# Kernel tuning notes

Hardware: AMD Instinct MI355X
Metric: run time of the kernel (lower is better)

Reference implementation:

```python
import jax, jax.numpy as jnp
import numpy as np

NUM_HEADS = 32
MULTI_HOP_MAX_DIST = 20


def setup_inputs() -> dict:
    key = jax.random.key(0)
    ks = jax.random.split(key, 10)
    B, N, D, F = 16, 64, 20, 3
    H = NUM_HEADS
    attn_bias = jax.random.normal(ks[0], (B, N + 1, N + 1), jnp.float32)
    spatial_pos = jax.random.randint(ks[1], (B, N, N), 0, 512)
    x = jax.random.randint(ks[2], (B, N, 9), 0, 512)
    edge_input = jax.random.randint(ks[3], (B, N, N, D, F), 0, 1536)
    attn_edge_type = jax.random.randint(ks[4], (B, N, N, F), 0, 1536)
    mask_2d = jnp.ones((B,), jnp.float32)
    edge_enc_w = (jax.random.normal(ks[5], (1537, H), jnp.float32) * 0.02).at[0].set(0.0)
    edge_dis_enc_w = jax.random.normal(ks[6], (131072, 1), jnp.float32) * 0.02
    spatial_enc_w = (jax.random.normal(ks[7], (512, H), jnp.float32) * 0.02).at[0].set(0.0)
    token_w = jax.random.normal(ks[8], (1, H), jnp.float32) * 0.02
    return {
        'attn_bias': attn_bias, 'spatial_pos': spatial_pos, 'x': x,
        'edge_input': edge_input, 'attn_edge_type': attn_edge_type,
        'mask_2d': mask_2d, 'edge_enc_w': edge_enc_w,
        'edge_dis_enc_w': edge_dis_enc_w, 'spatial_enc_w': spatial_enc_w,
        'token_w': token_w,
    }


def reference(attn_bias, spatial_pos, x, edge_input, attn_edge_type, mask_2d,
              edge_enc_w, edge_dis_enc_w, spatial_enc_w, token_w):
    H = NUM_HEADS
    D = MULTI_HOP_MAX_DIST
    B, N = x.shape[:2]

    # graph_attn_bias: [B, H, N+1, N+1]
    gab = jnp.tile(attn_bias[:, None], (1, H, 1, 1))

    # spatial position bias: gather + permute to [B, H, N, N]
    spb = jnp.transpose(spatial_enc_w[spatial_pos], (0, 3, 1, 2))
    spb = spb * mask_2d[:, None, None, None]
    gab = gab.at[:, :, 1:, 1:].add(spb)

    # virtual-distance token bias on graph-token row/col
    tok = token_w.reshape(1, H, 1)
    gab = gab.at[:, :, 1:, 0].add(tok)
    gab = gab.at[:, :, 0, :].add(tok)

    # spatial_pos_ = clamp(where(sp>1, sp-1, where(sp==0,1,sp)), 0, D)
    sp_ = jnp.where(spatial_pos == 0, 1, spatial_pos)
    sp_ = jnp.where(sp_ > 1, sp_ - 1, sp_)
    sp_ = jnp.clip(sp_, 0, D)

    # multi-hop edge features: [B,N,N,D,F] -> gather -> mean over F -> [B,N,N,D,H]
    ei = edge_input[:, :, :, :D, :]
    ef = edge_enc_w[ei].mean(-2)
    # per-distance head-mixing bmm: [D, B*N*N, H] x [D, H, H]
    flat = jnp.transpose(ef, (3, 0, 1, 2, 4)).reshape(D, -1, H)
    Wd = edge_dis_enc_w.reshape(-1, H, H)[:D]
    flat = jnp.matmul(flat, Wd)
    eb = jnp.transpose(flat.reshape(D, B, N, N, H), (1, 2, 3, 0, 4))
    eb = eb.sum(-2) / sp_.astype(jnp.float32)[..., None]  # [B,N,N,H]
    eb = jnp.transpose(eb, (0, 3, 1, 2)) * mask_2d[:, None, None, None]
    gab = gab.at[:, :, 1:, 1:].add(eb)

    return gab + attn_bias[:, None]
```

## Files before the change

### kernel.cpp

```cpp
#include <hip/hip_runtime.h>
#include <hip/hip_bf16.h>

#define NH 32
#define NV 1537
#define ND 20
#define NB 16
#define NN 64

#define ENCP_U32 (NV*10)
#define WD8_U32  (ND*NH*8)

#define CVT1_BLOCKS ((NV*8 + 255)/256)
#define CVT2_BLOCKS (WD8_U32/256)

#define MAIN_LDS 61480

typedef unsigned int   u32;
typedef unsigned short u16;
typedef __attribute__((ext_vector_type(4))) float        f32x4;
typedef __attribute__((ext_vector_type(4))) unsigned int u32x4;
typedef __attribute__((ext_vector_type(4))) int          v4i;

__device__ __forceinline__ u32 f32x4_to_fp8(float a0, float a1, float a2, float a3) {
#if __has_builtin(__builtin_amdgcn_cvt_pk_fp8_f32)
    u32 u = __builtin_amdgcn_cvt_pk_fp8_f32(a0, a1, 0u, false);
    u     = __builtin_amdgcn_cvt_pk_fp8_f32(a2, a3, u,  true);
    return u;
#else
    u32 lo, hi;
    asm("v_cvt_pk_fp8_f32 %0, %1, %2" : "=v"(lo) : "v"(a0), "v"(a1));
    asm("v_cvt_pk_fp8_f32 %0, %1, %2" : "=v"(hi) : "v"(a2), "v"(a3));
    return (lo & 0xffffu) | (hi << 16);
#endif
}

__global__ void __launch_bounds__(256)
prep_kernel(const float* __restrict__ enc,
            const float* __restrict__ wdis,
            u32* __restrict__ tab) {
    int blk = blockIdx.x, tid = threadIdx.x;
    if (blk < CVT1_BLOCKS) {
        int o = blk * 256 + tid;
        if (o < NV * 8) {
            float4 e = *(const float4*)(enc + (size_t)o * 4);
            tab[(o >> 3) * 10 + (o & 7)] = f32x4_to_fp8(e.x * 256.f, e.y * 256.f,
                                                        e.z * 256.f, e.w * 256.f);
        }
    } else {
        int o = (blk - CVT1_BLOCKS) * 256 + tid;
        int d = o >> 8, rem = o & 255;
        int h = rem >> 3, k4 = rem & 7;
        const float* ws = wdis + d * 1024 + h;
        tab[ENCP_U32 + (d * 32 + h) * 8 + k4] =
            f32x4_to_fp8(ws[(k4 * 4 + 0) * 32] * 256.f,
                         ws[(k4 * 4 + 1) * 32] * 256.f,
                         ws[(k4 * 4 + 2) * 32] * 256.f,
                         ws[(k4 * 4 + 3) * 32] * 256.f);
    }
}

__global__ void __launch_bounds__(512, 4)
main_kernel(const float* __restrict__ ab,
            const int*   __restrict__ spos,
            const int*   __restrict__ eidx,
            const float* __restrict__ mask2d,
            const float* __restrict__ spw,
            const float* __restrict__ tokw,
            const u32*   __restrict__ tab,
            float*       __restrict__ out) {
    extern __shared__ __align__(16) char dyn[];

    int tid = threadIdx.x, blk = blockIdx.x;
    int b = blk >> 5, i0 = (blk & 31) << 1;

    int wv = tid >> 6, l = tid & 63;
    int c16 = l & 15, g = l >> 4;
    int cellLoc = wv * 16 + c16;

    const int* ep = eidx + ((size_t)blk * 128 + cellLoc) * 60;
    u32 w[30];
#pragma unroll
    for (int k = 0; k < 15; ++k) {
        v4i q = *(const v4i*)(ep + k * 4);
        w[2 * k]     = ((u32)q.x & 0xffffu) | ((u32)q.y << 16);
        w[2 * k + 1] = ((u32)q.z & 0xffffu) | ((u32)q.w << 16);
    }

    {
        const u32x4* g4 = (const u32x4*)tab;
        u32x4* s4 = (u32x4*)dyn;
        for (int p = tid; p < 3842; p += 512) s4[p] = g4[p];
        if (tid < 2) ((u32*)dyn)[15368 + tid] = tab[15368 + tid];
    }
    __syncthreads();

    const char* encB = dyn + g * 8;
    const u32* wdg = tab + ENCP_U32;

    f32x4 acc[2][3] = {};

#pragma unroll
    for (int d = 0; d < ND; ++d) {
        u32 q0 = (w[(3 * d    ) >> 1] >> (((3 * d    ) & 1) * 16)) & 0xffffu;
        u32 q1 = (w[(3 * d + 1) >> 1] >> (((3 * d + 1) & 1) * 16)) & 0xffffu;
        u32 q2 = (w[(3 * d + 2) >> 1] >> (((3 * d + 2) & 1) * 16)) & 0xffffu;
        long bf0 = *(const long*)(wdg + (d * 32 + c16) * 8 + g * 2);
        long bf1 = *(const long*)(wdg + (d * 32 + c16 + 16) * 8 + g * 2);
        long a0 = *(const long*)(encB + q0 * 40u);
        long a1 = *(const long*)(encB + q1 * 40u);
        long a2 = *(const long*)(encB + q2 * 40u);
        acc[0][0] = __builtin_amdgcn_mfma_f32_16x16x32_fp8_fp8(a0, bf0, acc[0][0], 0, 0, 0);
        acc[1][0] = __builtin_amdgcn_mfma_f32_16x16x32_fp8_fp8(a0, bf1, acc[1][0], 0, 0, 0);
        acc[0][1] = __builtin_amdgcn_mfma_f32_16x16x32_fp8_fp8(a1, bf0, acc[0][1], 0, 0, 0);
        acc[1][1] = __builtin_amdgcn_mfma_f32_16x16x32_fp8_fp8(a1, bf1, acc[1][1], 0, 0, 0);
        acc[0][2] = __builtin_amdgcn_mfma_f32_16x16x32_fp8_fp8(a2, bf0, acc[0][2], 0, 0, 0);
        acc[1][2] = __builtin_amdgcn_mfma_f32_16x16x32_fp8_fp8(a2, bf1, acc[1][2], 0, 0, 0);
    }
    f32x4 acc0 = acc[0][0] + acc[0][1] + acc[0][2];
    f32x4 acc1 = acc[1][0] + acc[1][1] + acc[1][2];

    __syncthreads();
    float* comb = (float*)dyn;
    float m = mask2d[b];
#pragma unroll
    for (int r = 0; r < 4; ++r) {
        int cell = wv * 16 + g * 4 + r;
        int s = spos[blk * 128 + cell];
        int sp = (s == 0) ? 1 : s;
        sp = (sp > 1) ? sp - 1 : sp;
        sp = (sp > ND) ? ND : sp;
        float esc = m / (196608.0f * (float)sp);
        float spbL = spw[s * NH + c16];
        float spbH = spw[s * NH + c16 + 16];
        comb[cell * 33 + c16]      = spbL * m + acc0[r] * esc;
        comb[cell * 33 + c16 + 16] = spbH * m + acc1[r] * esc;
    }
    __syncthreads();

#pragma unroll
    for (int w8 = 0; w8 < 8; ++w8) {
        int idx = w8 * 512 + tid;
        int j = idx & 63, h = (idx >> 6) & 31, r = idx >> 11;
        float av = ab[(b * 65 + i0 + r + 1) * 65 + (j + 1)];
        __builtin_nontemporal_store(2.0f * av + comb[(r * 64 + j) * 33 + h],
            &out[(((size_t)b * NH + h) * 65 + i0 + r + 1) * 65 + (j + 1)]);
    }

    if (tid < 2 * NH) {
        int r = tid >> 5, h = tid & 31;
        float av0 = ab[(b * 65 + i0 + r + 1) * 65];
        __builtin_nontemporal_store(2.0f * av0 + tokw[h],
            &out[(((size_t)b * NH + h) * 65 + i0 + r + 1) * 65 + 0]);
    }
    if (i0 == 0) {
        for (int t = tid; t < NH * 65; t += 512) {
            int h = t / 65, j = t - h * 65;
            __builtin_nontemporal_store(2.0f * ab[b * 4225 + j] + tokw[h],
                &out[(((size_t)b * NH + h) * 65 + 0) * 65 + j]);
        }
    }
}

extern "C" void kernel_launch(void* const* d_in, const int* in_sizes, int n_in,
                              void* d_out, int out_size, void* d_ws, size_t ws_size,
                              hipStream_t stream) {
    const float* attn_bias   = (const float*)d_in[0];
    const int*   spatial_pos = (const int*)  d_in[1];
    const int*   edge_input  = (const int*)  d_in[3];
    const float* mask_2d     = (const float*)d_in[5];
    const float* edge_enc_w  = (const float*)d_in[6];
    const float* edge_dis_w  = (const float*)d_in[7];
    const float* spatial_w   = (const float*)d_in[8];
    const float* token_w     = (const float*)d_in[9];
    float* out = (float*)d_out;
    u32* tab = (u32*)d_ws;

    prep_kernel<<<CVT1_BLOCKS + CVT2_BLOCKS, 256, 0, stream>>>(
        edge_enc_w, edge_dis_w, tab);
    main_kernel<<<512, 512, MAIN_LDS, stream>>>(attn_bias, spatial_pos, edge_input,
                                                mask_2d, spatial_w, token_w,
                                                tab, out);
}
```

Baseline: 23.05 us.

## Drop LDS row padding, load edge indices in-loop, raise occupancy target

Stores the fp8 edge-encoding table with a dense 32-byte row stride instead of 40 bytes, which shrinks LDS per block and lets the row offset be computed with a shift. The up-front edge-index prefetch into 30 packed registers is removed; indices are now read from global memory inside the unrolled distance loop. Launch bounds are raised from 4 to 6 blocks per CU to trade registers for occupancy. Risks: a 32-byte stride can cause LDS bank conflicts on the gathers, and loading indices late exposes global memory latency right before each MFMA.

```diff
diff --git a/kernel.cpp b/kernel.cpp
--- a/kernel.cpp
+++ b/kernel.cpp
@@ -7,19 +7,18 @@
 #define NB 16
 #define NN 64
 
-#define ENCP_U32 (NV*10)
-#define WD8_U32  (ND*NH*8)
+#define ENC_U32 (NV*8)
+#define WD8_U32 (ND*NH*8)
 
-#define CVT1_BLOCKS ((NV*8 + 255)/256)
+#define CVT1_BLOCKS ((ENC_U32 + 255)/256)
 #define CVT2_BLOCKS (WD8_U32/256)
 
-#define MAIN_LDS 61480
+#define MAIN_LDS 49184
 
 typedef unsigned int   u32;
 typedef unsigned short u16;
 typedef __attribute__((ext_vector_type(4))) float        f32x4;
 typedef __attribute__((ext_vector_type(4))) unsigned int u32x4;
-typedef __attribute__((ext_vector_type(4))) int          v4i;
 
 __device__ __forceinline__ u32 f32x4_to_fp8(float a0, float a1, float a2, float a3) {
 #if __has_builtin(__builtin_amdgcn_cvt_pk_fp8_f32)
@@ -41,17 +40,17 @@
     int blk = blockIdx.x, tid = threadIdx.x;
     if (blk < CVT1_BLOCKS) {
         int o = blk * 256 + tid;
-        if (o < NV * 8) {
+        if (o < ENC_U32) {
             float4 e = *(const float4*)(enc + (size_t)o * 4);
-            tab[(o >> 3) * 10 + (o & 7)] = f32x4_to_fp8(e.x * 256.f, e.y * 256.f,
-                                                        e.z * 256.f, e.w * 256.f);
+            tab[o] = f32x4_to_fp8(e.x * 256.f, e.y * 256.f,
+                                  e.z * 256.f, e.w * 256.f);
         }
     } else {
         int o = (blk - CVT1_BLOCKS) * 256 + tid;
         int d = o >> 8, rem = o & 255;
         int h = rem >> 3, k4 = rem & 7;
         const float* ws = wdis + d * 1024 + h;
-        tab[ENCP_U32 + (d * 32 + h) * 8 + k4] =
+        tab[ENC_U32 + (d * 32 + h) * 8 + k4] =
             f32x4_to_fp8(ws[(k4 * 4 + 0) * 32] * 256.f,
                          ws[(k4 * 4 + 1) * 32] * 256.f,
                          ws[(k4 * 4 + 2) * 32] * 256.f,
@@ -59,7 +58,7 @@
     }
 }
 
-__global__ void __launch_bounds__(512, 4)
+__global__ void __launch_bounds__(512, 6)
 main_kernel(const float* __restrict__ ab,
             const int*   __restrict__ spos,
             const int*   __restrict__ eidx,
@@ -77,38 +76,29 @@
     int c16 = l & 15, g = l >> 4;
     int cellLoc = wv * 16 + c16;
 
-    const int* ep = eidx + ((size_t)blk * 128 + cellLoc) * 60;
-    u32 w[30];
-#pragma unroll
-    for (int k = 0; k < 15; ++k) {
-        v4i q = *(const v4i*)(ep + k * 4);
-        w[2 * k]     = ((u32)q.x & 0xffffu) | ((u32)q.y << 16);
-        w[2 * k + 1] = ((u32)q.z & 0xffffu) | ((u32)q.w << 16);
-    }
-
     {
         const u32x4* g4 = (const u32x4*)tab;
         u32x4* s4 = (u32x4*)dyn;
-        for (int p = tid; p < 3842; p += 512) s4[p] = g4[p];
-        if (tid < 2) ((u32*)dyn)[15368 + tid] = tab[15368 + tid];
+        for (int p = tid; p < 3074; p += 512) s4[p] = g4[p];
     }
     __syncthreads();
 
     const char* encB = dyn + g * 8;
-    const u32* wdg = tab + ENCP_U32;
+    const u32* wdg = tab + ENC_U32;
+    const int* ep = eidx + ((size_t)blk * 128 + cellLoc) * 60;
 
     f32x4 acc[2][3] = {};
 
 #pragma unroll
     for (int d = 0; d < ND; ++d) {
-        u32 q0 = (w[(3 * d    ) >> 1] >> (((3 * d    ) & 1) * 16)) & 0xffffu;
-        u32 q1 = (w[(3 * d + 1) >> 1] >> (((3 * d + 1) & 1) * 16)) & 0xffffu;
-        u32 q2 = (w[(3 * d + 2) >> 1] >> (((3 * d + 2) & 1) * 16)) & 0xffffu;
+        u32 q0 = (u32)ep[3 * d + 0];
+        u32 q1 = (u32)ep[3 * d + 1];
+        u32 q2 = (u32)ep[3 * d + 2];
         long bf0 = *(const long*)(wdg + (d * 32 + c16) * 8 + g * 2);
         long bf1 = *(const long*)(wdg + (d * 32 + c16 + 16) * 8 + g * 2);
-        long a0 = *(const long*)(encB + q0 * 40u);
-        long a1 = *(const long*)(encB + q1 * 40u);
-        long a2 = *(const long*)(encB + q2 * 40u);
+        long a0 = *(const long*)(encB + (q0 << 5));
+        long a1 = *(const long*)(encB + (q1 << 5));
+        long a2 = *(const long*)(encB + (q2 << 5));
         acc[0][0] = __builtin_amdgcn_mfma_f32_16x16x32_fp8_fp8(a0, bf0, acc[0][0], 0, 0, 0);
         acc[1][0] = __builtin_amdgcn_mfma_f32_16x16x32_fp8_fp8(a0, bf1, acc[1][0], 0, 0, 0);
         acc[0][1] = __builtin_amdgcn_mfma_f32_16x16x32_fp8_fp8(a1, bf0, acc[0][1], 0, 0, 0);
```

After: 24.77 us. 7.5% more time.
